# Optimization experiments

Measured on AMD Instinct MI355X. Metric: run time of the kernel, lower is better.

## Reference

```python
import jax, jax.numpy as jnp
import numpy as np

N_TOK = 384
VOCAB = 50000
N_POS = 52
WDIM = 512
HDIM = 1024
FEAT_DIM = 3 * 16  # np.repeat([len,start,end],16)


def setup_inputs() -> dict:
    key = jax.random.key(0)
    ks = jax.random.split(key, 10)
    s = 0.02  # init scale
    return {
        "sentence": jax.random.randint(ks[0], (N_TOK,), 0, VOCAB),
        "pos_tags": jax.random.randint(ks[1], (N_TOK,), 0, N_POS),
        "We_wrd": jax.random.normal(ks[2], (VOCAB, WDIM), jnp.float32) * s,
        "We_pos": jax.random.normal(ks[3], (N_POS, WDIM), jnp.float32) * s,
        "W_dan1": jax.random.normal(ks[4], (2 * WDIM, HDIM), jnp.float32) * s,
        "b_dan1": jnp.zeros((HDIM,), jnp.float32),
        "W_dan2": jax.random.normal(ks[5], (HDIM, HDIM), jnp.float32) * s,
        "b_dan2": jnp.zeros((HDIM,), jnp.float32),
        "W_s1": jax.random.normal(ks[6], (HDIM + FEAT_DIM, HDIM), jnp.float32) * s,
        "b_s1": jnp.zeros((HDIM,), jnp.float32),
        "W_s2": jax.random.normal(ks[7], (HDIM, 1), jnp.float32) * s,
        "b_s2": jnp.zeros((1,), jnp.float32),
    }


def reference(sentence, pos_tags, We_wrd, We_pos, W_dan1, b_dan1, W_dan2, b_dan2, W_s1, b_s1, W_s2, b_s2):
    n = sentence.shape[0]
    # per-token embedding: concat(pos, word) as in score() with use_pos=True -> [n, 2*wdim]
    emb = jnp.concatenate([We_pos[pos_tags], We_wrd[sentence]], axis=-1)
    # prefix sums so every span mean is O(1): pref[k] = sum of emb[:k]
    pref = jnp.concatenate([jnp.zeros((1, emb.shape[1]), emb.dtype), jnp.cumsum(emb, axis=0)], axis=0)
    # all spans (i, j) with i <= j, as in the double loop over i..n-1, j..n-1
    i_idx, j_idx = np.triu_indices(n)  # static shapes, S = n(n+1)/2
    i_idx = jnp.asarray(i_idx)
    j_idx = jnp.asarray(j_idx)
    end = j_idx + 1
    length = (end - i_idx).astype(emb.dtype)
    # DAN encoder: mean of span embeddings -> 2 relu layers (config['layer']=2)
    mean = (pref[end] - pref[i_idx]) / length[:, None]            # [S, 2*wdim]
    h = jax.nn.relu(mean @ W_dan1 + b_dan1)                        # [S, hdim]
    h = jax.nn.relu(h @ W_dan2 + b_dan2)                           # [S, hdim]
    # phrase feats: np.repeat([len, start, end], 16) -> [S, 48]
    feats = jnp.repeat(jnp.stack([length, i_idx.astype(emb.dtype), end.astype(emb.dtype)], axis=1), 16, axis=1)
    rep = jnp.concatenate([h, feats], axis=1)                      # [S, hdim+48]
    # Wpscore MLP: Linear(ph_dim+48 -> hdim) + relu, Linear(hdim -> 1)
    h2 = jax.nn.relu(rep @ W_s1 + b_s1)
    scores = (h2 @ W_s2 + b_s2)[:, 0]                              # [S]
    return scores
```

## Files before the change

### kernel.cpp

```cpp
#include <hip/hip_runtime.h>

#define NTOK  384
#define SPANS 73920
#define MPAD  74752
#define HD    1024
#define BK    32
#define KTS   (HD / BK)
#define GRID256 1168
#define CPX256  (GRID256 / 8)

typedef unsigned short u16;
typedef __attribute__((ext_vector_type(8))) short short8;
typedef __attribute__((ext_vector_type(4))) float floatx4;

#define VMCNT_IMM(N) (((N) & 0xF) | (((N) >> 4) << 14) | (0x7 << 4) | (0xF << 8))

__device__ __forceinline__ u16 f2bu(float x) {
  union { float f; unsigned u; } un; un.f = x;
  unsigned r = un.u + 0x7fffu + ((un.u >> 16) & 1u);
  return (u16)(r >> 16);
}

__device__ __forceinline__ void gld_lds16(const void* g, void* l) {
  __builtin_amdgcn_global_load_lds(
      (const __attribute__((address_space(1))) void*)g,
      (__attribute__((address_space(3))) void*)l, 16, 0, 0);
}

__global__ void emb_gather(const int* __restrict__ sent, const int* __restrict__ pos,
                           const float* __restrict__ Wwrd, const float* __restrict__ Wpos,
                           u16* __restrict__ embB) {
  int t = blockIdx.x;
  int c = threadIdx.x;
  int pt = pos[t], st = sent[t];
  #pragma unroll
  for (int u = 0; u < 4; ++u) {
    int col = u * 256 + c;
    float v = (col < 512) ? Wpos[(size_t)pt * 512 + col]
                          : Wwrd[(size_t)st * 512 + (col - 512)];
    embB[(size_t)t * HD + col] = f2bu(v);
  }
}

__global__ void prep_spans(int* __restrict__ spI, int* __restrict__ spE, float* __restrict__ spInv,
                           float* __restrict__ scores, const float* __restrict__ bs2) {
  int rf = blockIdx.x * 256 + threadIdx.x;
  if (rf >= MPAD) return;
  int s = rf < SPANS ? rf : SPANS - 1;
  const int n = NTOK;
  double tn = 2.0 * n + 1.0;
  int i = (int)((tn - sqrt(tn * tn - 8.0 * (double)s)) * 0.5);
  if (i < 0) i = 0;
  if (i > n - 1) i = n - 1;
  #define OFF(ii) (((ii) * (2 * n - (ii) + 1)) / 2)
  while (i + 1 <= n - 1 && OFF(i + 1) <= s) ++i;
  while (i > 0 && OFF(i) > s) --i;
  int j = i + (s - OFF(i));
  #undef OFF
  spI[rf] = i;
  spE[rf] = j + 1;
  spInv[rf] = 1.0f / (float)(j + 1 - i);
  if (rf < SPANS) scores[rf] = bs2[0];
}

__global__ void prep_castT(const float* __restrict__ Wd1, const float* __restrict__ Wd2,
                           const float* __restrict__ Ws1,
                           u16* __restrict__ o1, u16* __restrict__ o2, u16* __restrict__ o3) {
  int b = blockIdx.x;
  int w = b >> 10, rem = b & 1023;
  int tk = rem >> 5, tn = rem & 31;
  const float* src = (w == 0) ? Wd1 : ((w == 1) ? Wd2 : Ws1);
  u16* dst = (w == 0) ? o1 : ((w == 1) ? o2 : o3);
  __shared__ u16 tile[32][33];
  int x = threadIdx.x & 31, y = threadIdx.x >> 5;
  int k0 = tk * 32, n0 = tn * 32;
  for (int yy = 0; yy < 32; yy += 8)
    tile[y + yy][x] = f2bu(src[(size_t)(k0 + y + yy) * HD + n0 + x]);
  __syncthreads();
  for (int yy = 0; yy < 32; yy += 8)
    dst[(size_t)(n0 + y + yy) * HD + k0 + x] = tile[x][y + yy];
}

__global__ void prep_svec(const float* __restrict__ Ws1,
                          float* __restrict__ S0, float* __restrict__ S1v, float* __restrict__ S2v) {
  int c = blockIdx.x * 256 + threadIdx.x;
  if (c >= HD) return;
  float a = 0.f, b = 0.f, d = 0.f;
  for (int r = 0; r < 16; ++r) {
    a += Ws1[(size_t)(1024 + r) * HD + c];
    b += Ws1[(size_t)(1040 + r) * HD + c];
    d += Ws1[(size_t)(1056 + r) * HD + c];
  }
  S0[c] = a; S1v[c] = b; S2v[c] = d;
}

__global__ void yscan(const float* __restrict__ Y, float* __restrict__ Qp) {
  __shared__ float buf[NTOK];
  int c = blockIdx.x;
  int t = threadIdx.x;
  buf[t] = Y[(size_t)t * HD + c];
  __syncthreads();
  #pragma unroll
  for (int off = 1; off < NTOK; off <<= 1) {
    float add = (t >= off) ? buf[t - off] : 0.f;
    __syncthreads();
    buf[t] += add;
    __syncthreads();
  }
  if (t == 0) Qp[c] = 0.f;
  Qp[(size_t)(t + 1) * HD + c] = buf[t];
}

__global__ void expand(const float* __restrict__ Qp, const int* __restrict__ spI,
                       const int* __restrict__ spE, const float* __restrict__ spInv,
                       const float* __restrict__ b1, u16* __restrict__ out) {
  int gid = blockIdx.x * 256 + threadIdx.x;
  int row = gid >> 7;
  int c0 = (gid & 127) << 3;
  int i = spI[row], e = spE[row];
  float inv = spInv[row];
  const float* pe = Qp + (size_t)e * HD + c0;
  const float* pi = Qp + (size_t)i * HD + c0;
  const float* bb = b1 + c0;
  u16 tmp[8];
  #pragma unroll
  for (int u = 0; u < 8; ++u) {
    float v = (pe[u] - pi[u]) * inv + bb[u];
    v = v > 0.f ? v : 0.f;
    tmp[u] = f2bu(v);
  }
  *(uint4*)(out + (size_t)row * HD + c0) = *(const uint4*)tmp;
}

template <int EPI>
__global__ __launch_bounds__(256, 3) void gemm_bt(
    const u16* __restrict__ A, const u16* __restrict__ Bt,
    const float* __restrict__ bias, u16* __restrict__ C, float* __restrict__ Cf) {
  __shared__ u16 As[2][128 * BK];
  __shared__ u16 Bs[2][128 * BK];
  int bx = blockIdx.x;
  int nt = bx & 7, mt = bx >> 3;
  int m0 = mt * 128, n0 = nt * 128;
  int t = threadIdx.x, lane = t & 63, wid = t >> 6;
  int wm = wid >> 1, wn = wid & 1;
  int q = lane >> 4, r = lane & 15;

  floatx4 acc[4][4] = {};

  int dsub = (lane & 7) ^ ((lane >> 3) & 7);
  int row0 = wid * 16 + 2 * (lane >> 3) + (dsub >> 2);
  int voff = row0 * HD + (dsub & 3) * 8;
  const u16* gA0 = A  + (size_t)m0 * HD;
  const u16* gB0 = Bt + (size_t)n0 * HD;
  int ldsOff0 = wid * 512;
  int ldsOff1 = 2048 + wid * 512;

  auto stage = [&](int kt, int b) {
    const u16* pa = gA0 + voff + kt * BK;
    const u16* pb = gB0 + voff + kt * BK;
    gld_lds16(pa,                   &As[b][ldsOff0]);
    gld_lds16(pa + (size_t)64 * HD, &As[b][ldsOff1]);
    gld_lds16(pb,                   &Bs[b][ldsOff0]);
    gld_lds16(pb + (size_t)64 * HD, &Bs[b][ldsOff1]);
  };

  int oct = (((r & 1) << 2) + q) ^ ((r >> 1) & 7);
  int aoff[4], boff[4];
  #pragma unroll
  for (int x = 0; x < 4; ++x) {
    aoff[x] = (wm * 32 + x * 8 + (r >> 1)) * 64 + oct * 8;
    boff[x] = (wn * 32 + x * 8 + (r >> 1)) * 64 + oct * 8;
  }

  auto compute = [&](int b) {
    short8 af[4];
    #pragma unroll
    for (int x = 0; x < 4; ++x) af[x] = *(const short8*)(&As[b][aoff[x]]);
    #pragma unroll
    for (int ni = 0; ni < 4; ++ni) {
      short8 bf = *(const short8*)(&Bs[b][boff[ni]]);
      #pragma unroll
      for (int mi = 0; mi < 4; ++mi)
        acc[mi][ni] = __builtin_amdgcn_mfma_f32_16x16x32_bf16(af[mi], bf, acc[mi][ni], 0, 0, 0);
    }
  };

  stage(0, 0);
  #pragma unroll 1
  for (int kt = 0; kt < KTS; ++kt) {
    int cur = kt & 1;
    if (kt < KTS - 1) {
      stage(kt + 1, cur ^ 1);
      __builtin_amdgcn_s_waitcnt(VMCNT_IMM(4));
    } else {
      __builtin_amdgcn_s_waitcnt(VMCNT_IMM(0));
    }
    __builtin_amdgcn_s_barrier();
    compute(cur);
    __builtin_amdgcn_s_barrier();
  }

  #pragma unroll
  for (int mi = 0; mi < 4; ++mi) {
    int rowb = m0 + wm * 64 + mi * 16 + q * 4;
    #pragma unroll
    for (int ni = 0; ni < 4; ++ni) {
      int col = n0 + wn * 64 + ni * 16 + r;
      #pragma unroll
      for (int e = 0; e < 4; ++e)
        Cf[(size_t)(rowb + e) * HD + col] = acc[mi][ni][e];
    }
  }
}

template <int EPI>
__global__ __launch_bounds__(512, 2) void gemm256(
    const u16* __restrict__ A, const u16* __restrict__ Bt,
    const float* __restrict__ bias, u16* __restrict__ C,
    const int* __restrict__ spI, const int* __restrict__ spE,
    const float* __restrict__ S0, const float* __restrict__ S1v, const float* __restrict__ S2v,
    const float* __restrict__ Ws2, float* __restrict__ scores) {
  __shared__ u16 As[4][8192];
  __shared__ u16 Bs[4][8192];

  int swz = (blockIdx.x & 7) * CPX256 + (blockIdx.x >> 3);
  int mt = swz >> 2, nt = swz & 3;
  int m0 = mt * 256, n0 = nt * 256;
  int t = threadIdx.x, lane = t & 63, wid = t >> 6;
  int wm = wid >> 2, wn = wid & 3;
  int q = lane >> 4, r = lane & 15;

  floatx4 acc[8][4] = {};

  int dsub = (lane & 7) ^ ((lane >> 3) & 7);
  int row0 = wid * 16 + 2 * (lane >> 3) + (dsub >> 2);
  int voff = row0 * HD + (dsub & 3) * 8;
  const u16* gA0 = A  + (size_t)m0 * HD;
  const u16* gB0 = Bt + (size_t)n0 * HD;
  int ldsOff0 = wid * 512;
  int ldsOff1 = 4096 + wid * 512;

  auto stageA = [&](int kt) {
    int slot = kt & 3;
    const u16* pa = gA0 + voff + kt * BK;
    gld_lds16(pa,                    &As[slot][ldsOff0]);
    gld_lds16(pa + (size_t)128 * HD, &As[slot][ldsOff1]);
  };
  auto stageB = [&](int kt) {
    int slot = kt & 3;
    const u16* pb = gB0 + voff + kt * BK;
    gld_lds16(pb,                    &Bs[slot][ldsOff0]);
    gld_lds16(pb + (size_t)128 * HD, &Bs[slot][ldsOff1]);
  };

  int oct = (((r & 1) << 2) + q) ^ ((r >> 1) & 7);
  int aoff[8], boff[4];
  #pragma unroll
  for (int x = 0; x < 8; ++x) aoff[x] = (wm * 64 + x * 8 + (r >> 1)) * 64 + oct * 8;
  #pragma unroll
  for (int x = 0; x < 4; ++x) boff[x] = (wn * 32 + x * 8 + (r >> 1)) * 64 + oct * 8;

  stageA(0); stageB(0);
  stageA(1); stageB(1);
  stageA(2); stageB(2);
  __builtin_amdgcn_s_waitcnt(VMCNT_IMM(8));
  __builtin_amdgcn_s_barrier();

  #pragma unroll 1
  for (int kt = 0; kt < KTS; ++kt) {
    int slot = kt & 3;
    const u16* sA = As[slot];
    const u16* sB = Bs[slot];

    short8 af[4], bf[4];
    #pragma unroll
    for (int x = 0; x < 4; ++x) af[x] = *(const short8*)(sA + aoff[x]);
    #pragma unroll
    for (int x = 0; x < 4; ++x) bf[x] = *(const short8*)(sB + boff[x]);
    if (kt + 3 < KTS) stageA(kt + 3);
    __builtin_amdgcn_s_barrier();
    __builtin_amdgcn_s_setprio(1);
    #pragma unroll
    for (int ni = 0; ni < 4; ++ni)
      #pragma unroll
      for (int mi = 0; mi < 4; ++mi)
        acc[mi][ni] = __builtin_amdgcn_mfma_f32_16x16x32_bf16(af[mi], bf[ni], acc[mi][ni], 0, 0, 0);
    __builtin_amdgcn_s_setprio(0);
    __builtin_amdgcn_s_barrier();

    #pragma unroll
    for (int x = 0; x < 4; ++x) af[x] = *(const short8*)(sA + aoff[4 + x]);
    if (kt + 3 < KTS) stageB(kt + 3);
    if (kt < KTS - 3)       __builtin_amdgcn_s_waitcnt(VMCNT_IMM(8));
    else if (kt == KTS - 3) __builtin_amdgcn_s_waitcnt(VMCNT_IMM(4));
    else                    __builtin_amdgcn_s_waitcnt(VMCNT_IMM(0));
    __builtin_amdgcn_s_barrier();
    __builtin_amdgcn_s_setprio(1);
    #pragma unroll
    for (int ni = 0; ni < 4; ++ni)
      #pragma unroll
      for (int mi = 0; mi < 4; ++mi)
        acc[4 + mi][ni] = __builtin_amdgcn_mfma_f32_16x16x32_bf16(af[mi], bf[ni], acc[4 + mi][ni], 0, 0, 0);
    __builtin_amdgcn_s_setprio(0);
    __builtin_amdgcn_s_barrier();
  }

  if (EPI == 0) {
    #pragma unroll
    for (int ni = 0; ni < 4; ++ni) {
      int col = n0 + wn * 64 + ni * 16 + r;
      float bcol = bias[col];
      #pragma unroll
      for (int mi = 0; mi < 8; ++mi) {
        int rowb = m0 + wm * 128 + mi * 16 + q * 4;
        #pragma unroll
        for (int e = 0; e < 4; ++e) {
          float v = acc[mi][ni][e] + bcol;
          v = v > 0.f ? v : 0.f;
          C[(size_t)(rowb + e) * HD + col] = f2bu(v);
        }
      }
    }
  } else {
    float bcol[4], s0c[4], s1c[4], s2c[4], wsc[4];
    #pragma unroll
    for (int ni = 0; ni < 4; ++ni) {
      int col = n0 + wn * 64 + ni * 16 + r;
      bcol[ni] = bias[col]; s0c[ni] = S0[col]; s1c[ni] = S1v[col];
      s2c[ni] = S2v[col];  wsc[ni] = Ws2[col];
    }
    #pragma unroll
    for (int mi = 0; mi < 8; ++mi) {
      int rowb = m0 + wm * 128 + mi * 16 + q * 4;
      #pragma unroll
      for (int e = 0; e < 4; ++e) {
        int row = rowb + e;
        float fi = (float)spI[row];
        float fe = (float)spE[row];
        float fl = fe - fi;
        float p = 0.f;
        #pragma unroll
        for (int ni = 0; ni < 4; ++ni) {
          float v = acc[mi][ni][e] + bcol[ni] + fl * s0c[ni] + fi * s1c[ni] + fe * s2c[ni];
          v = v > 0.f ? v : 0.f;
          p += v * wsc[ni];
        }
        p += __shfl_xor(p, 1);
        p += __shfl_xor(p, 2);
        p += __shfl_xor(p, 4);
        p += __shfl_xor(p, 8);
        if (r == 0 && row < SPANS) atomicAdd(&scores[row], p);
      }
    }
  }
}

extern "C" void kernel_launch(void* const* d_in, const int* in_sizes, int n_in,
                              void* d_out, int out_size, void* d_ws, size_t ws_size,
                              hipStream_t stream) {
  const int*   sent = (const int*)d_in[0];
  const int*   pos  = (const int*)d_in[1];
  const float* Wwrd = (const float*)d_in[2];
  const float* Wpos = (const float*)d_in[3];
  const float* Wd1  = (const float*)d_in[4];
  const float* bd1  = (const float*)d_in[5];
  const float* Wd2  = (const float*)d_in[6];
  const float* bd2  = (const float*)d_in[7];
  const float* Ws1  = (const float*)d_in[8];
  const float* bs1  = (const float*)d_in[9];
  const float* Ws2  = (const float*)d_in[10];
  const float* bs2  = (const float*)d_in[11];
  float* scores = (float*)d_out;

  char* w = (char*)d_ws;
  size_t o = 0;
  auto alloc = [&](size_t bytes) {
    char* p = w + o;
    o = (o + bytes + 255) & ~(size_t)255;
    return p;
  };
  int*   spI   = (int*)  alloc((size_t)MPAD * 4);
  int*   spE   = (int*)  alloc((size_t)MPAD * 4);
  float* spInv = (float*)alloc((size_t)MPAD * 4);
  float* S0    = (float*)alloc(4096);
  float* S1v   = (float*)alloc(4096);
  float* S2v   = (float*)alloc(4096);
  u16*   embB  = (u16*)  alloc((size_t)NTOK * HD * 2);
  float* Ybuf  = (float*)alloc((size_t)NTOK * HD * 4);
  float* Qp    = (float*)alloc((size_t)(NTOK + 1) * HD * 4);
  u16* Wd1t = (u16*)alloc((size_t)HD * HD * 2);
  u16* Wd2t = (u16*)alloc((size_t)HD * HD * 2);
  u16* Ws1t = (u16*)alloc((size_t)HD * HD * 2);
  u16* bufA = (u16*)alloc((size_t)MPAD * HD * 2);
  u16* bufB = (u16*)alloc((size_t)MPAD * HD * 2);

  emb_gather<<<NTOK, 256, 0, stream>>>(sent, pos, Wwrd, Wpos, embB);
  prep_spans<<<(MPAD + 255) / 256, 256, 0, stream>>>(spI, spE, spInv, scores, bs2);
  prep_castT<<<3 * 1024, 256, 0, stream>>>(Wd1, Wd2, Ws1, Wd1t, Wd2t, Ws1t);
  prep_svec <<<4, 256, 0, stream>>>(Ws1, S0, S1v, S2v);

  gemm_bt<2><<<(NTOK / 128) * 8, 256, 0, stream>>>(embB, Wd1t, nullptr, nullptr, Ybuf);
  yscan<<<HD, NTOK, 0, stream>>>(Ybuf, Qp);
  expand<<<MPAD / 2, 256, 0, stream>>>(Qp, spI, spE, spInv, bd1, bufA);

  gemm256<0><<<GRID256, 512, 0, stream>>>(bufA, Wd2t, bd2, bufB,
                                          nullptr, nullptr, nullptr, nullptr, nullptr,
                                          nullptr, nullptr);
  gemm256<1><<<GRID256, 512, 0, stream>>>(bufB, Ws1t, bs1, nullptr,
                                          spI, spE, S0, S1v, S2v, Ws2, scores);
}
```

Baseline: 668.7 us.

## Restructure 256x256 GEMM main loop to BK=64 double-buffered half-tile staging

The bf16 256x256 GEMM kernel moves from a 4-slot ring of BK=32 tiles to 2 slots of BK=64 tiles. Each k-step is split into four phases that each stage a quarter tile (half of A or B) and run 16 MFMAs across two k-halves. A new XOR-swizzled LDS layout and per-k-half fragment offsets go with it. The aim is to halve the outer iterations and barrier count per unit of k and to overlap global-to-LDS loads more evenly with MFMA work. The cost is different register pressure from larger fragments and the risk of bank conflicts or wait-count mistakes in the new swizzle.

Result: slower. 685.0 us (+2.4%).

```diff
diff --git a/kernel.cpp b/kernel.cpp
--- a/kernel.cpp
+++ b/kernel.cpp
@@ -6,6 +6,8 @@
 #define HD    1024
 #define BK    32
 #define KTS   (HD / BK)
+#define BK64  64
+#define KT64  (HD / BK64)
 #define GRID256 1168
 #define CPX256  (GRID256 / 8)
 
@@ -220,8 +222,8 @@
     const int* __restrict__ spI, const int* __restrict__ spE,
     const float* __restrict__ S0, const float* __restrict__ S1v, const float* __restrict__ S2v,
     const float* __restrict__ Ws2, float* __restrict__ scores) {
-  __shared__ u16 As[4][8192];
-  __shared__ u16 Bs[4][8192];
+  __shared__ u16 As[2][16384];
+  __shared__ u16 Bs[2][16384];
 
   int swz = (blockIdx.x & 7) * CPX256 + (blockIdx.x >> 3);
   int mt = swz >> 2, nt = swz & 3;
@@ -232,77 +234,82 @@
 
   floatx4 acc[8][4] = {};
 
-  int dsub = (lane & 7) ^ ((lane >> 3) & 7);
-  int row0 = wid * 16 + 2 * (lane >> 3) + (dsub >> 2);
-  int voff = row0 * HD + (dsub & 3) * 8;
+  int clog = (lane & 7) ^ ((lane >> 3) & 7);
+  int gvoff = (wid * 8 + (lane >> 3)) * HD + clog * 8;
   const u16* gA0 = A  + (size_t)m0 * HD;
   const u16* gB0 = Bt + (size_t)n0 * HD;
-  int ldsOff0 = wid * 512;
-  int ldsOff1 = 4096 + wid * 512;
-
-  auto stageA = [&](int kt) {
-    int slot = kt & 3;
-    const u16* pa = gA0 + voff + kt * BK;
-    gld_lds16(pa,                    &As[slot][ldsOff0]);
-    gld_lds16(pa + (size_t)128 * HD, &As[slot][ldsOff1]);
+  int lw = wid * 512;
+
+  auto stage_half = [&](int s) {
+    int j = s >> 2, which = s & 3;
+    int slot = j & 1;
+    int rh = which & 1;
+    const u16* g = ((which < 2) ? gB0 : gA0) + (size_t)(rh * 128) * HD + j * 64 + gvoff;
+    u16* l = ((which < 2) ? Bs[slot] : As[slot]) + rh * 8192 + lw;
+    gld_lds16(g, l);
+    gld_lds16(g + (size_t)64 * HD, l + 4096);
   };
-  auto stageB = [&](int kt) {
-    int slot = kt & 3;
-    const u16* pb = gB0 + voff + kt * BK;
-    gld_lds16(pb,                    &Bs[slot][ldsOff0]);
-    gld_lds16(pb + (size_t)128 * HD, &Bs[slot][ldsOff1]);
-  };
-
-  int oct = (((r & 1) << 2) + q) ^ ((r >> 1) & 7);
-  int aoff[8], boff[4];
-  #pragma unroll
-  for (int x = 0; x < 8; ++x) aoff[x] = (wm * 64 + x * 8 + (r >> 1)) * 64 + oct * 8;
-  #pragma unroll
-  for (int x = 0; x < 4; ++x) boff[x] = (wn * 32 + x * 8 + (r >> 1)) * 64 + oct * 8;
-
-  stageA(0); stageB(0);
-  stageA(1); stageB(1);
-  stageA(2); stageB(2);
-  __builtin_amdgcn_s_waitcnt(VMCNT_IMM(8));
+
+  int aoff[8][2], boff[4][2];
+  #pragma unroll
+  for (int mi = 0; mi < 8; ++mi)
+    #pragma unroll
+    for (int kh = 0; kh < 2; ++kh)
+      aoff[mi][kh] = wm * 8192 + (mi * 16 + r) * 64 + (((q + 4 * kh) ^ (r & 7)) * 8);
+  #pragma unroll
+  for (int ni = 0; ni < 4; ++ni)
+    #pragma unroll
+    for (int kh = 0; kh < 2; ++kh)
+      boff[ni][kh] = (wn >> 1) * 8192 + ((wn & 1) * 64 + ni * 16 + r) * 64 +
+                     (((q + 4 * kh) ^ (r & 7)) * 8);
+
+  #pragma unroll
+  for (int s = 0; s < 6; ++s) stage_half(s);
+  __builtin_amdgcn_s_waitcnt(VMCNT_IMM(4));
   __builtin_amdgcn_s_barrier();
 
   #pragma unroll 1
-  for (int kt = 0; kt < KTS; ++kt) {
-    int slot = kt & 3;
+  for (int kt = 0; kt < KT64; ++kt) {
+    int slot = kt & 1;
     const u16* sA = As[slot];
     const u16* sB = Bs[slot];
-
-    short8 af[4], bf[4];
-    #pragma unroll
-    for (int x = 0; x < 4; ++x) af[x] = *(const short8*)(sA + aoff[x]);
-    #pragma unroll
-    for (int x = 0; x < 4; ++x) bf[x] = *(const short8*)(sB + boff[x]);
-    if (kt + 3 < KTS) stageA(kt + 3);
-    __builtin_amdgcn_s_barrier();
-    __builtin_amdgcn_s_setprio(1);
-    #pragma unroll
-    for (int ni = 0; ni < 4; ++ni)
-      #pragma unroll
-      for (int mi = 0; mi < 4; ++mi)
-        acc[mi][ni] = __builtin_amdgcn_mfma_f32_16x16x32_bf16(af[mi], bf[ni], acc[mi][ni], 0, 0, 0);
-    __builtin_amdgcn_s_setprio(0);
-    __builtin_amdgcn_s_barrier();
-
-    #pragma unroll
-    for (int x = 0; x < 4; ++x) af[x] = *(const short8*)(sA + aoff[4 + x]);
-    if (kt + 3 < KTS) stageB(kt + 3);
-    if (kt < KTS - 3)       __builtin_amdgcn_s_waitcnt(VMCNT_IMM(8));
-    else if (kt == KTS - 3) __builtin_amdgcn_s_waitcnt(VMCNT_IMM(4));
-    else                    __builtin_amdgcn_s_waitcnt(VMCNT_IMM(0));
-    __builtin_amdgcn_s_barrier();
-    __builtin_amdgcn_s_setprio(1);
-    #pragma unroll
-    for (int ni = 0; ni < 4; ++ni)
-      #pragma unroll
-      for (int mi = 0; mi < 4; ++mi)
-        acc[4 + mi][ni] = __builtin_amdgcn_mfma_f32_16x16x32_bf16(af[mi], bf[ni], acc[4 + mi][ni], 0, 0, 0);
-    __builtin_amdgcn_s_setprio(0);
-    __builtin_amdgcn_s_barrier();
+    int sbase = 4 * kt + 6;
+    short8 bf[4][2];
+
+    #pragma unroll
+    for (int p = 0; p < 4; ++p) {
+      short8 af[2][2];
+      #pragma unroll
+      for (int d = 0; d < 2; ++d)
+        #pragma unroll
+        for (int kh = 0; kh < 2; ++kh)
+          af[d][kh] = *(const short8*)(sA + aoff[2 * p + d][kh]);
+      if (p == 0) {
+        #pragma unroll
+        for (int ni = 0; ni < 4; ++ni)
+          #pragma unroll
+          for (int kh = 0; kh < 2; ++kh)
+            bf[ni][kh] = *(const short8*)(sB + boff[ni][kh]);
+      }
+      int s = sbase + p;
+      if (s < 4 * KT64) stage_half(s);
+      if (p == 3) {
+        if (kt < KT64 - 2) __builtin_amdgcn_s_waitcnt(VMCNT_IMM(4));
+        else               __builtin_amdgcn_s_waitcnt(VMCNT_IMM(0));
+      }
+      __builtin_amdgcn_s_barrier();
+      __builtin_amdgcn_s_setprio(1);
+      #pragma unroll
+      for (int kh = 0; kh < 2; ++kh)
+        #pragma unroll
+        for (int ni = 0; ni < 4; ++ni)
+          #pragma unroll
+          for (int d = 0; d < 2; ++d)
+            acc[2 * p + d][ni] = __builtin_amdgcn_mfma_f32_16x16x32_bf16(
+                af[d][kh], bf[ni][kh], acc[2 * p + d][ni], 0, 0, 0);
+      __builtin_amdgcn_s_setprio(0);
+      __builtin_amdgcn_s_barrier();
+    }
   }
 
   if (EPI == 0) {
```
